# Kernel optimization log

Measured on AMD Instinct MI355X. Metric: run time of the kernel, lower is better.

Reference implementation:

```python
import jax, jax.numpy as jnp
import numpy as np

B, L, D_SEQ, D_GLOBAL = 32, 2048, 1024, 1024
H, DK, DV = 16, 64, 64


def setup_inputs() -> dict:
    key = jax.random.key(0)
    k1, k2, k3, k4, k5 = jax.random.split(key, 5)
    scale = 0.05
    return {
        "X": jax.random.normal(k1, (B, D_GLOBAL), dtype=jnp.float32),
        "S": jax.random.normal(k2, (B, L, D_SEQ), dtype=jnp.float32),
        "Wq": jax.random.normal(k3, (H, D_GLOBAL, DK), dtype=jnp.float32) * scale,
        "Wk": jax.random.normal(k4, (H, D_SEQ, DK), dtype=jnp.float32) * scale,
        "Wv": jax.random.normal(k5, (H, D_SEQ, DV), dtype=jnp.float32) * scale,
    }


def reference(X, S, Wq, Wk, Wv):
    # X: [B, d_global], S: [B, L, d_seq]
    d_key = Wq.shape[-1]
    inv_sqrt_dk = 1.0 / jnp.sqrt(jnp.float32(d_key))
    # Values: gelu (exact, erf-based like tf default) projection -> [B, H, L, DV]
    VS = jax.nn.gelu(jnp.einsum("bld,hdv->bhlv", S, Wv), approximate=False)
    # Single global query per head: tanh projection -> [B, H, DK]
    Q = jnp.tanh(jnp.einsum("bd,hdk->bhk", X, Wq))
    # Keys: tanh projection -> [B, H, L, DK]
    KS = jnp.tanh(jnp.einsum("bld,hdk->bhlk", S, Wk))
    # Attention logits (batched GEMV): [B, H, L]
    logits = jnp.einsum("bhk,bhlk->bhl", Q, KS) * inv_sqrt_dk
    Z = jax.nn.softmax(logits, axis=-1)
    # Weighted sum of values: [B, H, DV] -> flatten to [B, H*DV]
    Y = jnp.einsum("bhl,bhlv->bhv", Z, VS)
    return Y.reshape(Y.shape[0], -1)
```

## Files before the change

kernel.cpp:

```cpp
#include <hip/hip_runtime.h>
#include <math.h>

#define B_   32
#define L_   2048
#define DSEQ 1024
#define DGLB 1024
#define H_   16
#define DK_  64
#define DV_  64
#define LT   64
#define NT   (L_/LT)
#define PSTRIDE 66

#define WC_KSTRIDE 4096
#define WC_HSTRIDE 131072

#define AS1 __attribute__((address_space(1)))
#define AS3 __attribute__((address_space(3)))

using u16    = unsigned short;
using bf16x8 = __attribute__((ext_vector_type(8))) short;
using f32x4  = __attribute__((ext_vector_type(4))) float;

__device__ __forceinline__ u16 f2bf(float x) {
  union { float f; unsigned int u; } v; v.f = x;
  return (u16)((v.u + 0x7fffu + ((v.u >> 16) & 1u)) >> 16);
}

__device__ __forceinline__ float tanh_fast(float x) {
  float e = __builtin_exp2f(x * 2.885390081777927f);
  return 1.f - 2.f/(e + 1.f);
}

__device__ __forceinline__ float erf_fast(float x) {
  float ax = fabsf(x);
  float t  = 1.f/(1.f + 0.3275911f*ax);
  float p  = t*(0.254829592f + t*(-0.284496736f + t*(1.421413741f +
             t*(-1.453152027f + t*1.061405429f))));
  float e  = __builtin_exp2f(-ax*ax*1.4426950408889634f);
  float r  = 1.f - p*e;
  return copysignf(r, x);
}

__global__ void pack_w_kernel(const float* __restrict__ Wk,
                              const float* __restrict__ Wv,
                              u16* __restrict__ Wc) {
  const int h = blockIdx.x, j = blockIdx.y;
  const float* src = (j < DK_) ? (Wk + (size_t)h*DSEQ*DK_ + j)
                               : (Wv + (size_t)h*DSEQ*DV_ + (j - DK_));
  u16* dst = Wc + (size_t)h*WC_HSTRIDE + (size_t)j*32;
  for (int d = threadIdx.x; d < DSEQ; d += blockDim.x)
    dst[(size_t)(d >> 5)*WC_KSTRIDE + (d & 31)] = f2bf(src[(size_t)d*64]);
}

__global__ void s2bf_kernel(const float* __restrict__ S, u16* __restrict__ Sb) {
  const size_t G = (size_t)B_*L_*DSEQ/8;
  for (size_t i = (size_t)blockIdx.x*256 + threadIdx.x; i < G; i += (size_t)4096*256) {
    const float4* sp = (const float4*)(S + i*8);
    float4 v0 = sp[0], v1 = sp[1];
    bf16x8 wv;
    wv[0]=(short)f2bf(v0.x); wv[1]=(short)f2bf(v0.y);
    wv[2]=(short)f2bf(v0.z); wv[3]=(short)f2bf(v0.w);
    wv[4]=(short)f2bf(v1.x); wv[5]=(short)f2bf(v1.y);
    wv[6]=(short)f2bf(v1.z); wv[7]=(short)f2bf(v1.w);
    *(bf16x8*)(Sb + i*8) = wv;
  }
}

__global__ void q_proj_kernel(const float* __restrict__ X,
                              const float* __restrict__ Wq,
                              float* __restrict__ Q) {
  const int h = blockIdx.x, b0 = blockIdx.y*4, k = threadIdx.x;
  const float* w = Wq + (size_t)h*DGLB*DK_ + k;
  float a0=0.f, a1=0.f, a2=0.f, a3=0.f;
  for (int d = 0; d < DGLB; ++d) {
    float wv = w[(size_t)d*DK_];
    a0 += X[(size_t)(b0+0)*DGLB + d]*wv;
    a1 += X[(size_t)(b0+1)*DGLB + d]*wv;
    a2 += X[(size_t)(b0+2)*DGLB + d]*wv;
    a3 += X[(size_t)(b0+3)*DGLB + d]*wv;
  }
  Q[((size_t)(b0+0)*H_+h)*DK_+k] = tanhf(a0);
  Q[((size_t)(b0+1)*H_+h)*DK_+k] = tanhf(a1);
  Q[((size_t)(b0+2)*H_+h)*DK_+k] = tanhf(a2);
  Q[((size_t)(b0+3)*H_+h)*DK_+k] = tanhf(a3);
}

template<int BF16SRC>
__global__ __launch_bounds__(256, 3) void fused_kernel(
    const float* __restrict__ S, const u16* __restrict__ Sb,
    const u16* __restrict__ Wc, const float* __restrict__ Q,
    float* __restrict__ part) {
  __shared__ u16   Slds[2*64*128];
  __shared__ float lpart[2][64];

  const int id   = blockIdx.x;
  const int slot = id & 7;
  const int m    = id >> 3;
  const int tile = (m + (slot << 7)) & 1023;
  const int t    = tile & (NT-1), b = tile >> 5;

  const int tid  = threadIdx.x;
  const int wave = tid >> 6, lane = tid & 63;
  const int lhi  = lane >> 4, llo = lane & 15;
  const int isV  = wave & 1,  hp  = wave >> 1;
  const int h    = slot*2 + hp;

  const u16* wb = Wc + (size_t)h*WC_HSTRIDE + (size_t)(isV*64 + llo)*32 + lhi*8;
  int arow[4];
  #pragma unroll
  for (int rt = 0; rt < 4; ++rt) arow[rt] = (rt*16 + llo)*256;

  const u16*   Sv = Sb + ((size_t)b*L_ + (size_t)t*LT)*DSEQ;
  const float* Sf = S  + ((size_t)b*L_ + (size_t)t*LT)*DSEQ;

  auto stage_gl = [&](int sub) {
    const int bs = (sub & 1) * 8192;
    #pragma unroll
    for (int it = 0; it < 4; ++it) {
      const int j   = wave*4 + it;
      const int row = 4*j + (lane >> 4);
      const int g   = (lane & 15) ^ (row & 15);
      const u16* gp = Sv + (size_t)row*DSEQ + sub*128 + (g << 3);
      __builtin_amdgcn_global_load_lds(
          (const AS1 void*)gp, (AS3 void*)(Slds + bs + j*512), 16, 0, 0);
    }
  };
  auto stage_reg = [&](int sub) {
    const int bs = (sub & 1) * 16384;
    #pragma unroll
    for (int it = 0; it < 4; ++it) {
      int f = it*256 + tid, row = f >> 4, q = f & 15;
      int g = q ^ (row & 15);
      const float4* sp = (const float4*)(Sf + (size_t)row*DSEQ + sub*128 + g*8);
      float4 v0 = sp[0], v1 = sp[1];
      bf16x8 wv;
      wv[0]=(short)f2bf(v0.x); wv[1]=(short)f2bf(v0.y);
      wv[2]=(short)f2bf(v0.z); wv[3]=(short)f2bf(v0.w);
      wv[4]=(short)f2bf(v1.x); wv[5]=(short)f2bf(v1.y);
      wv[6]=(short)f2bf(v1.z); wv[7]=(short)f2bf(v1.w);
      *(bf16x8*)((char*)Slds + bs + row*256 + q*16) = wv;
    }
  };

  f32x4 acc[4][4];
  #pragma unroll
  for (int rt = 0; rt < 4; ++rt)
    #pragma unroll
    for (int c = 0; c < 4; ++c) acc[rt][c] = {0.f,0.f,0.f,0.f};

  bf16x8 bA[4], bB[4], bC[4], bD[4];
  if (BF16SRC) stage_gl(0);
  #pragma unroll
  for (int c = 0; c < 4; ++c) bA[c] = *(const bf16x8*)(wb + (size_t)0*WC_KSTRIDE + c*512);
  #pragma unroll
  for (int c = 0; c < 4; ++c) bB[c] = *(const bf16x8*)(wb + (size_t)1*WC_KSTRIDE + c*512);
  #pragma unroll
  for (int c = 0; c < 4; ++c) bC[c] = *(const bf16x8*)(wb + (size_t)2*WC_KSTRIDE + c*512);
  #pragma unroll
  for (int c = 0; c < 4; ++c) bD[c] = *(const bf16x8*)(wb + (size_t)3*WC_KSTRIDE + c*512);
  if (BF16SRC) __syncthreads();

#define KSTEP(BUF, kk)                                                        \
  do {                                                                        \
    const int colb = (((kk)*4 + lhi) ^ llo) << 4;                             \
    __builtin_amdgcn_s_setprio(1);                                            \
    _Pragma("unroll")                                                         \
    for (int rt = 0; rt < 4; ++rt) {                                          \
      bf16x8 af = *(const bf16x8*)(cb + arow[rt] + colb);                     \
      acc[rt][0] = __builtin_amdgcn_mfma_f32_16x16x32_bf16(af, BUF[0], acc[rt][0], 0,0,0); \
      acc[rt][1] = __builtin_amdgcn_mfma_f32_16x16x32_bf16(af, BUF[1], acc[rt][1], 0,0,0); \
      acc[rt][2] = __builtin_amdgcn_mfma_f32_16x16x32_bf16(af, BUF[2], acc[rt][2], 0,0,0); \
      acc[rt][3] = __builtin_amdgcn_mfma_f32_16x16x32_bf16(af, BUF[3], acc[rt][3], 0,0,0); \
    }                                                                         \
    __builtin_amdgcn_s_setprio(0);                                            \
    {                                                                         \
      const int kn = (s*4 + (kk) + 4) & 31;                                   \
      _Pragma("unroll")                                                       \
      for (int c = 0; c < 4; ++c)                                             \
        BUF[c] = *(const bf16x8*)(wb + (size_t)kn*WC_KSTRIDE + c*512);        \
    }                                                                         \
  } while (0)

  #pragma unroll
  for (int s = 0; s < 8; ++s) {
    if (BF16SRC) {
      if (s < 7) stage_gl(s + 1);
    } else {
      stage_reg(s);
      __syncthreads();
    }
    const char* cb = (const char*)Slds + (s & 1)*16384;
    KSTEP(bA, 0); KSTEP(bB, 1); KSTEP(bC, 2); KSTEP(bD, 3);
    __syncthreads();
  }
#undef KSTEP

  if (!isV) {
    const float* Qb = Q + ((size_t)b*H_ + h)*DK_;
    float q[4];
    #pragma unroll
    for (int c = 0; c < 4; ++c) q[c] = Qb[16*c + llo];
    #pragma unroll
    for (int rt = 0; rt < 4; ++rt) {
      #pragma unroll
      for (int r = 0; r < 4; ++r) {
        float pl = q[0]*tanh_fast(acc[rt][0][r]) + q[1]*tanh_fast(acc[rt][1][r])
                 + q[2]*tanh_fast(acc[rt][2][r]) + q[3]*tanh_fast(acc[rt][3][r]);
        pl += __shfl_xor(pl, 1); pl += __shfl_xor(pl, 2);
        pl += __shfl_xor(pl, 4); pl += __shfl_xor(pl, 8);
        if (llo == 0) lpart[hp][rt*16 + lhi*4 + r] = pl;
      }
    }
  } else {
    #pragma unroll
    for (int rt = 0; rt < 4; ++rt)
      #pragma unroll
      for (int c = 0; c < 4; ++c)
        #pragma unroll
        for (int r = 0; r < 4; ++r) {
          float x = acc[rt][c][r];
          acc[rt][c][r] = 0.5f*x*(1.f + erf_fast(x*0.70710678118654752f));
        }
  }
  __syncthreads();

  if (isV) {
    float lg = lpart[hp][lane] * 0.125f;
    float mx = lg;
    #pragma unroll
    for (int mk = 1; mk < 64; mk <<= 1) mx = fmaxf(mx, __shfl_xor(mx, mk));
    float ev = __expf(lg - mx);
    float sv = ev;
    #pragma unroll
    for (int mk = 1; mk < 64; mk <<= 1) sv += __shfl_xor(sv, mk);

    float er[16];
    #pragma unroll
    for (int rt = 0; rt < 4; ++rt)
      #pragma unroll
      for (int r = 0; r < 4; ++r)
        er[rt*4 + r] = __shfl(ev, rt*16 + lhi*4 + r);

    float* pt = part + (((size_t)b*H_ + h)*NT + t)*PSTRIDE;
    #pragma unroll
    for (int c = 0; c < 4; ++c) {
      float y = 0.f;
      #pragma unroll
      for (int rt = 0; rt < 4; ++rt)
        #pragma unroll
        for (int r = 0; r < 4; ++r)
          y += er[rt*4 + r]*acc[rt][c][r];
      y += __shfl_xor(y, 16); y += __shfl_xor(y, 32);
      if (lhi == 0) pt[2 + 16*c + llo] = y;
    }
    if (lane == 0) { pt[0] = mx; pt[1] = sv; }
  }
}

__global__ void finalize_kernel(const float* __restrict__ part,
                                float* __restrict__ out) {
  const int h = blockIdx.x, b = blockIdx.y, v = threadIdx.x;
  const float* p = part + ((size_t)b*H_ + h)*(size_t)NT*PSTRIDE;
  float M = -3.0e38f;
  for (int tt = 0; tt < NT; ++tt) M = fmaxf(M, p[tt*PSTRIDE]);
  float ss = 0.f, y = 0.f;
  for (int tt = 0; tt < NT; ++tt) {
    float w = expf(p[tt*PSTRIDE] - M);
    ss += w*p[tt*PSTRIDE + 1];
    y  += w*p[tt*PSTRIDE + 2 + v];
  }
  out[((size_t)b*H_ + h)*DV_ + v] = y/ss;
}

extern "C" void kernel_launch(void* const* d_in, const int* in_sizes, int n_in,
                              void* d_out, int out_size, void* d_ws, size_t ws_size,
                              hipStream_t stream) {
  const float* X  = (const float*)d_in[0];
  const float* S  = (const float*)d_in[1];
  const float* Wq = (const float*)d_in[2];
  const float* Wk = (const float*)d_in[3];
  const float* Wv = (const float*)d_in[4];
  float* out = (float*)d_out;

  char* ws = (char*)d_ws;
  u16*   Wc    = (u16*)ws;
  float* Qbuf  = (float*)(ws + (4u<<20));
  float* part  = (float*)(ws + (4u<<20) + (128u<<10));
  u16*   Sb    = (u16*)(ws + (16u<<20));
  const bool useBf = ws_size >= (144ull << 20);

  pack_w_kernel  <<<dim3(H_, 128),  256, 0, stream>>>(Wk, Wv, Wc);
  q_proj_kernel  <<<dim3(H_, B_/4),  64, 0, stream>>>(X, Wq, Qbuf);
  if (useBf) {
    s2bf_kernel         <<<dim3(4096), 256, 0, stream>>>(S, Sb);
    fused_kernel<1>     <<<dim3(NT*B_*8), 256, 0, stream>>>(S, Sb, Wc, Qbuf, part);
  } else {
    fused_kernel<0>     <<<dim3(NT*B_*8), 256, 0, stream>>>(S, Sb, Wc, Qbuf, part);
  }
  finalize_kernel<<<dim3(H_, B_),    64, 0, stream>>>(part, out);
}
```

Baseline: 460.5 us.

## Triple-buffer LDS staging with partial vmcnt waits instead of full syncthreads

Moves the S-tile LDS staging from double to triple buffering, prefetching two sub-tiles ahead. Full __syncthreads after each K chunk is replaced by a barrier that waits only on enough outstanding vector-memory ops to guarantee the needed buffer landed, using explicit vmcnt counts and sched_barriers. The weight pointer now advances incrementally rather than being recomputed. This keeps more global loads in flight across K steps, at the cost of 50% more LDS (which may reduce occupancy) and hand-tuned vmcnt counts that are fragile if the compiler reorders loads. The last iteration (s==7) skips the barrier.

```diff
diff --git a/kernel.cpp b/kernel.cpp
--- a/kernel.cpp
+++ b/kernel.cpp
@@ -41,6 +41,14 @@
   float r  = 1.f - p*e;
   return copysignf(r, x);
 }
+
+#define PHASE_BARRIER(N)                                   \
+  do {                                                     \
+    __builtin_amdgcn_sched_barrier(0);                     \
+    asm volatile("s_waitcnt vmcnt(" #N ")" ::: "memory");  \
+    __builtin_amdgcn_s_barrier();                          \
+    __builtin_amdgcn_sched_barrier(0);                     \
+  } while (0)
 
 __global__ void pack_w_kernel(const float* __restrict__ Wk,
                               const float* __restrict__ Wv,
@@ -91,7 +99,7 @@
     const float* __restrict__ S, const u16* __restrict__ Sb,
     const u16* __restrict__ Wc, const float* __restrict__ Q,
     float* __restrict__ part) {
-  __shared__ u16   Slds[2*64*128];
+  __shared__ u16   Slds[3*64*128];
   __shared__ float lpart[2][64];
 
   const int id   = blockIdx.x;
@@ -115,7 +123,7 @@
   const float* Sf = S  + ((size_t)b*L_ + (size_t)t*LT)*DSEQ;
 
   auto stage_gl = [&](int sub) {
-    const int bs = (sub & 1) * 8192;
+    const int bs = (sub % 3) * 8192;
     #pragma unroll
     for (int it = 0; it < 4; ++it) {
       const int j   = wave*4 + it;
@@ -127,7 +135,7 @@
     }
   };
   auto stage_reg = [&](int sub) {
-    const int bs = (sub & 1) * 16384;
+    const int bs = (sub % 3) * 16384;
     #pragma unroll
     for (int it = 0; it < 4; ++it) {
       int f = it*256 + tid, row = f >> 4, q = f & 15;
@@ -149,8 +157,12 @@
     #pragma unroll
     for (int c = 0; c < 4; ++c) acc[rt][c] = {0.f,0.f,0.f,0.f};
 
+  if (BF16SRC) {
+    stage_gl(0);
+    stage_gl(1);
+    __builtin_amdgcn_sched_barrier(0);
+  }
   bf16x8 bA[4], bB[4], bC[4], bD[4];
-  if (BF16SRC) stage_gl(0);
   #pragma unroll
   for (int c = 0; c < 4; ++c) bA[c] = *(const bf16x8*)(wb + (size_t)0*WC_KSTRIDE + c*512);
   #pragma unroll
@@ -159,7 +171,8 @@
   for (int c = 0; c < 4; ++c) bC[c] = *(const bf16x8*)(wb + (size_t)2*WC_KSTRIDE + c*512);
   #pragma unroll
   for (int c = 0; c < 4; ++c) bD[c] = *(const bf16x8*)(wb + (size_t)3*WC_KSTRIDE + c*512);
-  if (BF16SRC) __syncthreads();
+  const u16* wbp = wb + (size_t)4*WC_KSTRIDE;
+  if (BF16SRC) PHASE_BARRIER(20);
 
 #define KSTEP(BUF, kk)                                                        \
   do {                                                                        \
@@ -174,25 +187,29 @@
       acc[rt][3] = __builtin_amdgcn_mfma_f32_16x16x32_bf16(af, BUF[3], acc[rt][3], 0,0,0); \
     }                                                                         \
     __builtin_amdgcn_s_setprio(0);                                            \
-    {                                                                         \
-      const int kn = (s*4 + (kk) + 4) & 31;                                   \
-      _Pragma("unroll")                                                       \
-      for (int c = 0; c < 4; ++c)                                             \
-        BUF[c] = *(const bf16x8*)(wb + (size_t)kn*WC_KSTRIDE + c*512);        \
-    }                                                                         \
+    _Pragma("unroll")                                                         \
+    for (int c = 0; c < 4; ++c)                                               \
+      BUF[c] = *(const bf16x8*)(wbp + c*512);                                 \
+    wbp += ((s*4 + (kk) + 4) == 31) ? -(ptrdiff_t)(31*WC_KSTRIDE)             \
+                                    : (ptrdiff_t)WC_KSTRIDE;                  \
   } while (0)
 
   #pragma unroll
   for (int s = 0; s < 8; ++s) {
     if (BF16SRC) {
-      if (s < 7) stage_gl(s + 1);
+      if (s < 6) { stage_gl(s + 2); __builtin_amdgcn_sched_barrier(0); }
     } else {
       stage_reg(s);
       __syncthreads();
     }
-    const char* cb = (const char*)Slds + (s & 1)*16384;
+    const char* cb = (const char*)Slds + (s % 3)*16384;
     KSTEP(bA, 0); KSTEP(bB, 1); KSTEP(bC, 2); KSTEP(bD, 3);
-    __syncthreads();
+    if (BF16SRC) {
+      if (s < 6)       PHASE_BARRIER(36);
+      else if (s == 6) PHASE_BARRIER(32);
+    } else {
+      __syncthreads();
+    }
   }
 #undef KSTEP
 
```

New measurement: 460.8 us. About the same (+0.0%).
